# Kernel optimization log

Hardware: AMD Instinct MI355X
Metric: run time of the kernel (lower is better)

Reference implementation:

```python
import jax, jax.numpy as jnp
import numpy as np

N_NODES = 100000
N_EDGES = 1600000
N_REL = 8      # num_node_types in the torch module, used as relation count
D_IN = 128
D_HID = 128
D_OUT = 64


def setup_inputs() -> dict:
    key = jax.random.key(0)
    ks = jax.random.split(key, 16)
    x = jax.random.normal(ks[0], (N_NODES, D_IN), dtype=jnp.float32)
    edge_index = jax.random.randint(ks[1], (2, N_EDGES), 0, N_NODES, dtype=jnp.int64)
    edge_type = jax.random.randint(ks[2], (N_EDGES,), 0, N_REL, dtype=jnp.int64)
    # Glorot-ish init scale for stability
    def w(k, shape):
        fan = shape[-2] + shape[-1]
        return jax.random.normal(k, shape, dtype=jnp.float32) * jnp.sqrt(2.0 / fan)
    params = {
        'Wrel1': w(ks[3], (N_REL, D_IN, D_HID)),  'Wroot1': w(ks[4], (D_IN, D_HID)),  'b1': jnp.zeros((D_HID,), jnp.float32),
        'Wrel2': w(ks[5], (N_REL, D_HID, D_HID)), 'Wroot2': w(ks[6], (D_HID, D_HID)), 'b2': jnp.zeros((D_HID,), jnp.float32),
        'Wrel3': w(ks[7], (N_REL, D_HID, D_OUT)), 'Wroot3': w(ks[8], (D_HID, D_OUT)), 'b3': jnp.zeros((D_OUT,), jnp.float32),
    }
    return {'x': x, 'edge_index': edge_index, 'edge_type': edge_type, **params}


def _rgcn_conv(x, src, dst, edge_type, Wrel, Wroot, b):
    # Per-relation transform of all nodes: [R, N, out] (small GEMMs),
    # then per-edge gather + scatter-add (the memory-bound part).
    h = jnp.einsum('ni,rio->rno', x, Wrel)          # [R, N, out]
    msgs = h[edge_type, src]                        # [E, out] irregular gather
    agg = jax.ops.segment_sum(msgs, dst, num_segments=x.shape[0])  # [N, out]
    return x @ Wroot + b + agg


def reference(x, edge_index, edge_type, Wrel1, Wroot1, b1, Wrel2, Wroot2, b2, Wrel3, Wroot3, b3):
    src, dst = edge_index[0], edge_index[1]
    # Dropout is identity in eval mode (training=False in the torch module).
    h = jax.nn.relu(_rgcn_conv(x, src, dst, edge_type, Wrel1, Wroot1, b1))
    h = jax.nn.relu(_rgcn_conv(h, src, dst, edge_type, Wrel2, Wroot2, b2))
    h = _rgcn_conv(h, src, dst, edge_type, Wrel3, Wroot3, b3)
    return jax.nn.log_softmax(h, axis=-1)
```

## Files before the change

kernel.cpp:

```cpp
#include <hip/hip_runtime.h>


#define DEVI __device__ __forceinline__

typedef __attribute__((ext_vector_type(8))) short bf16x8;
typedef __attribute__((ext_vector_type(4))) float f32x4;

DEVI unsigned short f2b(float f) {
  unsigned int u = __builtin_bit_cast(unsigned int, f);
  unsigned int r = (u + 0x7FFFu + ((u >> 16) & 1u)) >> 16;
  return (unsigned short)r;
}
DEVI float b2f(unsigned short h) {
  unsigned int u = ((unsigned int)h) << 16;
  return __builtin_bit_cast(float, u);
}
DEVI float lo16f(unsigned v) { return __builtin_bit_cast(float, v << 16); }
DEVI float hi16f(unsigned v) { return __builtin_bit_cast(float, v & 0xFFFF0000u); }
DEVI int imin(int a, int b) { return a < b ? a : b; }


__global__ void k_zero2(int* __restrict__ cnt, int n) {
  int stride = gridDim.x * blockDim.x;
  for (int i = blockIdx.x * blockDim.x + threadIdx.x; i < n; i += stride) cnt[i] = 0;
}

__global__ void k_chist(const int* __restrict__ et, const int* __restrict__ edst,
                        int* __restrict__ gh, int NG, int E) {
  __shared__ int h[128];
  if (threadIdx.x < 128) h[threadIdx.x] = 0;
  __syncthreads();
  int stride = gridDim.x * blockDim.x;
  for (int i = blockIdx.x * blockDim.x + threadIdx.x; i < E; i += stride)
    atomicAdd(&h[(et[i] & 7) * NG + (edst[i] >> 13)], 1);
  __syncthreads();
  if (threadIdx.x < 128) atomicAdd(&gh[threadIdx.x], h[threadIdx.x]);
}

__global__ void k_cscan(const int* __restrict__ gh, int* __restrict__ gcursor,
                        int* __restrict__ cbase, int NBC, int E) {
  if (threadIdx.x == 0) {
    int a = 0;
    for (int b = 0; b < NBC; ++b) { cbase[b] = a; gcursor[b] = a; a += gh[b]; }
    cbase[NBC] = E;
  }
}

__launch_bounds__(256)
__global__ void k_cfill(const int* __restrict__ et, const int* __restrict__ esrc,
                        const int* __restrict__ edst, int* __restrict__ gcursor,
                        int* __restrict__ stage, int NG, int E) {
  __shared__ int h[128], base[128], lc[128];
  int nb = gridDim.x;
  int slice = (E + nb - 1) / nb;
  int lo = blockIdx.x * slice;
  int hi = lo + slice < E ? lo + slice : E;
  int t = threadIdx.x;
  if (t < 128) { h[t] = 0; lc[t] = 0; }
  __syncthreads();
  for (int i = lo + t; i < hi; i += 256)
    atomicAdd(&h[(et[i] & 7) * NG + (edst[i] >> 13)], 1);
  __syncthreads();
  if (t < 128 && h[t] > 0) base[t] = atomicAdd(&gcursor[t], h[t]);
  __syncthreads();
  for (int i = lo + t; i < hi; i += 256) {
    int d = edst[i];
    int tile = d >> 6;
    int bin = (et[i] & 7) * NG + (tile >> 7);
    int p = base[bin] + atomicAdd(&lc[bin], 1);
    stage[p] = ((tile & 127) << 23) | ((d & 63) << 17) | esrc[i];
  }
}

__launch_bounds__(1024)
__global__ void k_fine(const int* __restrict__ cbase, const int* __restrict__ stage,
                       int* __restrict__ srcl, int* __restrict__ lo9,
                       int* __restrict__ len9, int NG, int NTr) {
  __shared__ int h[8192];
  __shared__ int tsum[1024];
  __shared__ int wsum[16];
  int b = blockIdx.x;
  int rel = b / NG, tg = b - rel * NG;
  int lo = cbase[b], hi = cbase[b + 1];
  int t = threadIdx.x;
  for (int k = t; k < 8192; k += 1024) h[k] = 0;
  __syncthreads();
  for (int i = lo + t; i < hi; i += 1024)
    atomicAdd(&h[(stage[i] >> 17) & 0x1FFF], 1);
  __syncthreads();
  int dbase = tg * 8192;
  size_t relbase = (size_t)rel * NTr;
  for (int k = t; k < 8192; k += 1024) {
    int d = dbase + k;
    if (d < NTr) len9[relbase + d] = h[k];
  }
  int loc[8];
  int s = 0;
  int kb = t * 8;
#pragma unroll
  for (int j = 0; j < 8; ++j) { loc[j] = s; s += h[kb + j]; }
  tsum[t] = s;
  __syncthreads();
  int lane = t & 63, w = t >> 6;
  int v = tsum[t];
#pragma unroll
  for (int o = 1; o < 64; o <<= 1) {
    int u = __shfl_up(v, o);
    if (lane >= o) v += u;
  }
  if (lane == 63) wsum[w] = v;
  __syncthreads();
  if (t == 0) {
    int a = 0;
#pragma unroll
    for (int j = 0; j < 16; ++j) { int tmp = wsum[j]; wsum[j] = a; a += tmp; }
  }
  __syncthreads();
  int texcl = v - s + wsum[w];
#pragma unroll
  for (int j = 0; j < 8; ++j) h[kb + j] = texcl + loc[j];
  __syncthreads();
  for (int k = t; k < 8192; k += 1024) {
    int d = dbase + k;
    if (d < NTr) lo9[relbase + d] = lo + h[k];
  }
  __syncthreads();
  for (int i = lo + t; i < hi; i += 1024) {
    int pk = stage[i];
    int key = (pk >> 17) & 0x1FFF;
    int p = atomicAdd(&h[key], 1);
    srcl[lo + p] = pk & 0x1FFFF;
  }
}


__global__ void wprep_kernel(const float* __restrict__ Wrel, const float* __restrict__ Wroot,
                             unsigned short* __restrict__ wt, int DOUT) {
  int total = 9 * 128 * DOUT;
  int stride = gridDim.x * blockDim.x;
  for (int i = blockIdx.x * blockDim.x + threadIdx.x; i < total; i += stride) {
    int k = i & 127;
    int oo = i >> 7;
    int o = oo % DOUT;
    int rr = oo / DOUT;
    float v = (rr < 8) ? Wrel[((size_t)rr * 128 + k) * DOUT + o]
                       : Wroot[(size_t)k * DOUT + o];
    wt[i] = f2b(v);
  }
}


template <int NRP>
__launch_bounds__(256)
__global__ void agg_kernel(const unsigned* __restrict__ x32,
                           const int* __restrict__ lo9, const int* __restrict__ len9,
                           const int* __restrict__ srcl,
                           unsigned* __restrict__ Ydw,
                           int r0, int N, int E, int NTr) {
  int lane = threadIdx.x & 63;
  int d = (blockIdx.x * blockDim.x + threadIdx.x) >> 6;
  if (d >= N) return;

  int lo[NRP], ln[NRP];
#pragma unroll
  for (int r = 0; r < NRP; ++r) {
    size_t idx = (size_t)(r0 + r) * NTr + d;
    lo[r] = lo9[idx];
    ln[r] = len9[idx];
  }

  int s0[NRP], s1[NRP];
#pragma unroll
  for (int r = 0; r < NRP; ++r) {
    s0[r] = srcl[imin(lo[r], E - 1)];
    s1[r] = srcl[imin(lo[r] + 1, E - 1)];
  }
  unsigned v0[NRP], v1[NRP];
#pragma unroll
  for (int r = 0; r < NRP; ++r) {
    v0[r] = x32[(size_t)s0[r] * 64 + lane];
    v1[r] = x32[(size_t)s1[r] * 64 + lane];
  }

#pragma unroll
  for (int r = 0; r < NRP; ++r) {
    float a0 = 0.f, a1 = 0.f;
    if (ln[r] > 0) { a0 += lo16f(v0[r]); a1 += hi16f(v0[r]); }
    if (ln[r] > 1) { a0 += lo16f(v1[r]); a1 += hi16f(v1[r]); }
    if (ln[r] > 2) {
      int i = lo[r] + 2, e = lo[r] + ln[r];
      for (; i + 2 <= e; i += 2) {
        int sA = srcl[i], sB = srcl[i + 1];
        unsigned vA = x32[(size_t)sA * 64 + lane];
        unsigned vB = x32[(size_t)sB * 64 + lane];
        a0 += lo16f(vA) + lo16f(vB);
        a1 += hi16f(vA) + hi16f(vB);
      }
      if (i < e) {
        unsigned vA = x32[(size_t)srcl[i] * 64 + lane];
        a0 += lo16f(vA);
        a1 += hi16f(vA);
      }
    }
    Ydw[(size_t)d * (NRP * 64) + r * 64 + lane] =
        (unsigned)f2b(a0) | ((unsigned)f2b(a1) << 16);
  }
}


struct SrcArr {
  const unsigned short* a[9];
  const unsigned short* w[9];
  int st[9];
};

template <int DOUT, int NK, int EPI>
__launch_bounds__(256)
__global__ void gemm_lds(SrcArr S, const float* __restrict__ bias,
                         const unsigned short* __restrict__ part,
                         unsigned short* __restrict__ out_b,
                         float* __restrict__ out_f, int N) {
  __shared__ unsigned short Al[2][64 * 128];
  constexpr int NF = (DOUT == 128) ? 2 : 1;
  int tid = threadIdx.x, wid = tid >> 6, lane = tid & 63;
  int colb = lane & 15, kgrp = lane >> 4;
  int colw = wid * 16 * NF;
  int tilebase = blockIdx.x * 64;

  auto stage = [&](int t, int buf) {
    const unsigned short* sa = S.a[t] + (size_t)tilebase * S.st[t];
    int st = S.st[t];
#pragma unroll
    for (int q = 0; q < 4; ++q) {
      int c = q * 256 + tid;
      int row = c >> 4, kcl = c & 15;
      int kcg = kcl ^ (row & 7);
      const unsigned short* gp = sa + (size_t)row * st + kcg * 8;
      unsigned short* lp = &Al[buf][(q * 256 + (tid & ~63)) * 8];
      __builtin_amdgcn_global_load_lds(
          (__attribute__((address_space(1))) void*)gp,
          (__attribute__((address_space(3))) void*)lp, 16, 0, 0);
    }
  };

  f32x4 acc[4][NF];
#pragma unroll
  for (int rb = 0; rb < 4; ++rb)
#pragma unroll
    for (int nf = 0; nf < NF; ++nf) {
      f32x4 z = {0.f, 0.f, 0.f, 0.f};
      acc[rb][nf] = z;
    }

  stage(0, 0);
#pragma unroll
  for (int t = 0; t < NK; ++t) {
    __syncthreads();
    if (t + 1 < NK) stage(t + 1, (t + 1) & 1);
    const unsigned short* W = S.w[t];
    const unsigned short* Ab = Al[t & 1];
#pragma unroll
    for (int kk = 0; kk < 4; ++kk) {
      int kc = kk * 4 + kgrp;
      bf16x8 a[4];
#pragma unroll
      for (int rb = 0; rb < 4; ++rb) {
        int arow = rb * 16 + colb;
        a[rb] = *(const bf16x8*)(Ab + (size_t)(arow * 16 + (kc ^ (arow & 7))) * 8);
      }
#pragma unroll
      for (int nf = 0; nf < NF; ++nf) {
        bf16x8 b = *(const bf16x8*)(W + (size_t)(colw + nf * 16 + colb) * 128 + kc * 8);
#pragma unroll
        for (int rb = 0; rb < 4; ++rb)
          acc[rb][nf] = __builtin_amdgcn_mfma_f32_16x16x32_bf16(a[rb], b, acc[rb][nf], 0, 0, 0);
      }
    }
  }

  float bv[NF];
  if (EPI == 0 || EPI == 3 || EPI == 4) {
#pragma unroll
    for (int nf = 0; nf < NF; ++nf) bv[nf] = bias[colw + nf * 16 + colb];
  }

  if ((EPI == 2 || EPI == 4) && DOUT == 64) {
    float* Lf = (float*)Al;
    __syncthreads();
#pragma unroll
    for (int rb = 0; rb < 4; ++rb)
#pragma unroll
      for (int i = 0; i < 4; ++i) {
        int row = rb * 16 + kgrp * 4 + i;
        int grow = tilebase + row;
        int rc = grow < N ? grow : 0;
        float v = acc[rb][0][i];
        if (EPI == 4) v += bv[0];
        else v += b2f(part[(size_t)rc * 64 + colw + colb]);
        Lf[row * 68 + colw + colb] = v;
      }
    __syncthreads();
#pragma unroll
    for (int it = 0; it < 4; ++it) {
      int row = wid * 16 + it * 4 + (lane >> 4);
      float v[4];
#pragma unroll
      for (int j = 0; j < 4; ++j) v[j] = Lf[row * 68 + colb + j * 16];
      float m = fmaxf(fmaxf(v[0], v[1]), fmaxf(v[2], v[3]));
#pragma unroll
      for (int s = 1; s < 16; s <<= 1) m = fmaxf(m, __shfl_xor(m, s));
      float sum = 0.f;
#pragma unroll
      for (int j = 0; j < 4; ++j) sum += __expf(v[j] - m);
#pragma unroll
      for (int s = 1; s < 16; s <<= 1) sum += __shfl_xor(sum, s);
      float lse = m + __logf(sum);
      int grow = tilebase + row;
      if (grow < N) {
#pragma unroll
        for (int j = 0; j < 4; ++j)
          out_f[(size_t)grow * 64 + colb + j * 16] = v[j] - lse;
      }
    }
  } else {
#pragma unroll
    for (int rb = 0; rb < 4; ++rb)
#pragma unroll
      for (int i = 0; i < 4; ++i) {
        int row = tilebase + rb * 16 + kgrp * 4 + i;
        bool ok = row < N;
        int rc = ok ? row : 0;
#pragma unroll
        for (int nf = 0; nf < NF; ++nf) {
          int col = colw + nf * 16 + colb;
          float v = acc[rb][nf][i];
          if (EPI == 0 || EPI == 3) v += bv[nf];
          if (EPI == 1 || EPI == 5) v += b2f(part[(size_t)rc * DOUT + col]);
          if (EPI == 1 || EPI == 3) v = fmaxf(v, 0.f);
          if (ok) out_b[(size_t)row * DOUT + col] = f2b(v);
        }
      }
  }
}

template <int DOUT>
static void run_gemm(int NK, int EPI, const SrcArr& S, const float* bias,
                     const unsigned short* part, unsigned short* ob, float* of,
                     int N, int NT, hipStream_t st) {
#define GCALL(nk, epi)                                                        \
  if (NK == nk && EPI == epi) {                                               \
    gemm_lds<DOUT, nk, epi><<<NT, 256, 0, st>>>(S, bias, part, ob, of, N);    \
    return;                                                                   \
  }
  GCALL(9, 3) GCALL(9, 4)
  GCALL(5, 0) GCALL(4, 1) GCALL(4, 2)
  GCALL(3, 0) GCALL(2, 5) GCALL(2, 1) GCALL(2, 2)
#undef GCALL
}


__global__ void cast_kernel(const float* __restrict__ in, unsigned short* __restrict__ out,
                            int n4) {
  int stride = gridDim.x * blockDim.x;
  for (int i = blockIdx.x * blockDim.x + threadIdx.x; i < n4; i += stride) {
    float4 v = ((const float4*)in)[i];
    ushort4 o;
    o.x = f2b(v.x); o.y = f2b(v.y); o.z = f2b(v.z); o.w = f2b(v.w);
    ((ushort4*)out)[i] = o;
  }
}


extern "C" void kernel_launch(void* const* d_in, const int* in_sizes, int n_in,
                              void* d_out, int out_size, void* d_ws, size_t ws_size,
                              hipStream_t stream) {
  const float* x = (const float*)d_in[0];
  const int* eidx = (const int*)d_in[1];
  const int* et = (const int*)d_in[2];
  const float* Wrel1 = (const float*)d_in[3];
  const float* Wroot1 = (const float*)d_in[4];
  const float* b1 = (const float*)d_in[5];
  const float* Wrel2 = (const float*)d_in[6];
  const float* Wroot2 = (const float*)d_in[7];
  const float* b2 = (const float*)d_in[8];
  const float* Wrel3 = (const float*)d_in[9];
  const float* Wroot3 = (const float*)d_in[10];
  const float* b3 = (const float*)d_in[11];

  const int N = in_sizes[0] / 128;
  const int E = in_sizes[2];
  const int NT = (N + 63) / 64;
  const int NTr = NT * 64;
  const int NG = (NT + 127) / 128;
  const int NBC = 8 * NG;
  const int* esrc = eidx;
  const int* edst = eidx + E;

  const size_t XB = (size_t)NTr * 128 * 2;

  size_t fixedB = 2 * XB + 2 * ((size_t)9 * 128 * 128 * 2) + (size_t)9 * 64 * 128 * 2 +
                  2 * ((size_t)E * 4) + 2 * ((size_t)8 * NTr * 4) + 4096 + 16 * 256;
  int NRP = 8;
  if (fixedB + 8 * XB > ws_size) NRP = 4;
  if (NRP == 4 && fixedB + 4 * XB + XB > ws_size) NRP = 2;

  char* p = (char*)d_ws;
  auto carve = [&](size_t bytes) {
    void* q = (void*)p;
    p += (bytes + 255) & ~(size_t)255;
    return q;
  };
  unsigned short* bufX0 = (unsigned short*)carve(XB);
  unsigned short* bufX1 = (unsigned short*)carve(XB);
  unsigned short* wt1 = (unsigned short*)carve((size_t)9 * 128 * 128 * 2);
  unsigned short* wt2 = (unsigned short*)carve((size_t)9 * 128 * 128 * 2);
  unsigned short* wt3 = (unsigned short*)carve((size_t)9 * 64 * 128 * 2);
  int* stage = (int*)carve((size_t)E * 4);
  int* srcl = (int*)carve((size_t)E * 4);
  int* lo9 = (int*)carve((size_t)8 * NTr * 4);
  int* len9 = (int*)carve((size_t)8 * NTr * 4);
  int* gh = (int*)carve(512);
  int* gcursor = (int*)carve(512);
  int* cbase = (int*)carve(512);
  unsigned short* part = (unsigned short*)((NRP < 8) ? carve(XB) : nullptr);
  unsigned short* Y = (unsigned short*)carve((size_t)NRP * XB);

  k_zero2<<<1, 128, 0, stream>>>(gh, 128);
  k_chist<<<512, 256, 0, stream>>>(et, edst, gh, NG, E);
  k_cscan<<<1, 64, 0, stream>>>(gh, gcursor, cbase, NBC, E);
  k_cfill<<<512, 256, 0, stream>>>(et, esrc, edst, gcursor, stage, NG, E);
  k_fine<<<NBC, 1024, 0, stream>>>(cbase, stage, srcl, lo9, len9, NG, NTr);

  wprep_kernel<<<576, 256, 0, stream>>>(Wrel1, Wroot1, wt1, 128);
  wprep_kernel<<<576, 256, 0, stream>>>(Wrel2, Wroot2, wt2, 128);
  wprep_kernel<<<288, 256, 0, stream>>>(Wrel3, Wroot3, wt3, 64);
  cast_kernel<<<2048, 256, 0, stream>>>(x, bufX0, N * 128 / 4);

  const int ablk = (N * 64 + 255) / 256;
  const int passes = 8 / NRP;

  auto layer = [&](const unsigned short* xin, const unsigned short* wt,
                   const float* bias, int DOUT, unsigned short* xout, float* fout) {
    for (int pidx = 0; pidx < passes; ++pidx) {
      int r0 = pidx * NRP;
      if (NRP == 8)
        agg_kernel<8><<<ablk, 256, 0, stream>>>((const unsigned*)xin, lo9, len9, srcl, (unsigned*)Y, r0, N, E, NTr);
      else if (NRP == 4)
        agg_kernel<4><<<ablk, 256, 0, stream>>>((const unsigned*)xin, lo9, len9, srcl, (unsigned*)Y, r0, N, E, NTr);
      else
        agg_kernel<2><<<ablk, 256, 0, stream>>>((const unsigned*)xin, lo9, len9, srcl, (unsigned*)Y, r0, N, E, NTr);

      SrcArr S;
      int idx = 0;
      if (pidx == 0) {
        S.a[0] = xin; S.w[0] = wt + (size_t)8 * DOUT * 128; S.st[0] = 128;
        idx = 1;
      }
      for (int j = 0; j < NRP; ++j) {
        S.a[idx] = Y + j * 128;
        S.w[idx] = wt + (size_t)(r0 + j) * DOUT * 128;
        S.st[idx] = NRP * 128;
        ++idx;
      }
      int NK = idx;
      int epi;
      bool lastp = (pidx == passes - 1);
      if (pidx == 0 && lastp) epi = (DOUT == 64) ? 4 : 3;
      else if (pidx == 0) epi = 0;
      else if (!lastp) epi = 5;
      else epi = (DOUT == 64) ? 2 : 1;

      unsigned short* ob = lastp ? xout : part;
      if (pidx == 0 && !lastp) ob = part;
      if (DOUT == 128)
        run_gemm<128>(NK, epi, S, bias, part, ob, fout, N, NT, stream);
      else
        run_gemm<64>(NK, epi, S, bias, part, ob, fout, N, NT, stream);
    }
  };

  layer(bufX0, wt1, b1, 128, bufX1, nullptr);
  layer(bufX1, wt2, b2, 128, bufX0, nullptr);
  layer(bufX0, wt3, b3, 64, nullptr, (float*)d_out);
}
```

Baseline: 694.4 us.

## Fuse per-relation gather aggregation into the GEMM kernel per layer

Replaces the separate aggregation kernel, which wrote per-relation sums Y to global memory, and the multi-input GEMM with one fused kernel per layer. Each block aggregates one relation's neighbor sums for its 64-row tile into LDS and then runs the MFMA step for that relation, overlapping the next relation's first gathers with the current MFMA. This removes the round trip of the large Y buffer through global memory and the partial-sum passes. In exchange, occupancy and memory-level parallelism drop: each wave handles 16 rows serially with a per-edge loop, and about 36 KB of LDS per block limits residency.

Result: slower. 801.0 us (+15.4%).

```diff
diff --git a/kernel.cpp b/kernel.cpp
--- a/kernel.cpp
+++ b/kernel.cpp
@@ -150,98 +150,50 @@
 }
 
 
-template <int NRP>
+template <int DOUT, bool LSM>
 __launch_bounds__(256)
-__global__ void agg_kernel(const unsigned* __restrict__ x32,
-                           const int* __restrict__ lo9, const int* __restrict__ len9,
-                           const int* __restrict__ srcl,
-                           unsigned* __restrict__ Ydw,
-                           int r0, int N, int E, int NTr) {
-  int lane = threadIdx.x & 63;
-  int d = (blockIdx.x * blockDim.x + threadIdx.x) >> 6;
-  if (d >= N) return;
-
-  int lo[NRP], ln[NRP];
-#pragma unroll
-  for (int r = 0; r < NRP; ++r) {
-    size_t idx = (size_t)(r0 + r) * NTr + d;
-    lo[r] = lo9[idx];
-    ln[r] = len9[idx];
-  }
-
-  int s0[NRP], s1[NRP];
-#pragma unroll
-  for (int r = 0; r < NRP; ++r) {
-    s0[r] = srcl[imin(lo[r], E - 1)];
-    s1[r] = srcl[imin(lo[r] + 1, E - 1)];
-  }
-  unsigned v0[NRP], v1[NRP];
-#pragma unroll
-  for (int r = 0; r < NRP; ++r) {
-    v0[r] = x32[(size_t)s0[r] * 64 + lane];
-    v1[r] = x32[(size_t)s1[r] * 64 + lane];
-  }
-
-#pragma unroll
-  for (int r = 0; r < NRP; ++r) {
-    float a0 = 0.f, a1 = 0.f;
-    if (ln[r] > 0) { a0 += lo16f(v0[r]); a1 += hi16f(v0[r]); }
-    if (ln[r] > 1) { a0 += lo16f(v1[r]); a1 += hi16f(v1[r]); }
-    if (ln[r] > 2) {
-      int i = lo[r] + 2, e = lo[r] + ln[r];
-      for (; i + 2 <= e; i += 2) {
-        int sA = srcl[i], sB = srcl[i + 1];
-        unsigned vA = x32[(size_t)sA * 64 + lane];
-        unsigned vB = x32[(size_t)sB * 64 + lane];
-        a0 += lo16f(vA) + lo16f(vB);
-        a1 += hi16f(vA) + hi16f(vB);
-      }
-      if (i < e) {
-        unsigned vA = x32[(size_t)srcl[i] * 64 + lane];
-        a0 += lo16f(vA);
-        a1 += hi16f(vA);
-      }
-    }
-    Ydw[(size_t)d * (NRP * 64) + r * 64 + lane] =
-        (unsigned)f2b(a0) | ((unsigned)f2b(a1) << 16);
-  }
-}
-
-
-struct SrcArr {
-  const unsigned short* a[9];
-  const unsigned short* w[9];
-  int st[9];
-};
-
-template <int DOUT, int NK, int EPI>
-__launch_bounds__(256)
-__global__ void gemm_lds(SrcArr S, const float* __restrict__ bias,
-                         const unsigned short* __restrict__ part,
-                         unsigned short* __restrict__ out_b,
-                         float* __restrict__ out_f, int N) {
-  __shared__ unsigned short Al[2][64 * 128];
+__global__ void fused_layer(const unsigned short* __restrict__ xb,
+                            const unsigned short* __restrict__ wt,
+                            const int* __restrict__ lo9,
+                            const int* __restrict__ len9,
+                            const int* __restrict__ srcl,
+                            const float* __restrict__ bias,
+                            unsigned short* __restrict__ out_b,
+                            float* __restrict__ out_f,
+                            int N, int NTr, int E) {
+  __shared__ unsigned short XY[2 * 64 * 128];
+  __shared__ int ll0[512], ll1[512];
+  unsigned short* Xl = XY;
+  unsigned short* Yl = XY + 8192;
   constexpr int NF = (DOUT == 128) ? 2 : 1;
   int tid = threadIdx.x, wid = tid >> 6, lane = tid & 63;
   int colb = lane & 15, kgrp = lane >> 4;
   int colw = wid * 16 * NF;
   int tilebase = blockIdx.x * 64;
-
-  auto stage = [&](int t, int buf) {
-    const unsigned short* sa = S.a[t] + (size_t)tilebase * S.st[t];
-    int st = S.st[t];
+  const unsigned* x32 = (const unsigned*)xb;
+
+  {
+    const unsigned short* sa = xb + (size_t)tilebase * 128;
 #pragma unroll
     for (int q = 0; q < 4; ++q) {
       int c = q * 256 + tid;
       int row = c >> 4, kcl = c & 15;
       int kcg = kcl ^ (row & 7);
-      const unsigned short* gp = sa + (size_t)row * st + kcg * 8;
-      unsigned short* lp = &Al[buf][(q * 256 + (tid & ~63)) * 8];
+      const unsigned short* gp = sa + (size_t)row * 128 + kcg * 8;
+      unsigned short* lp = &Xl[(q * 256 + (tid & ~63)) * 8];
       __builtin_amdgcn_global_load_lds(
           (__attribute__((address_space(1))) void*)gp,
           (__attribute__((address_space(3))) void*)lp, 16, 0, 0);
     }
-  };
+  }
+#pragma unroll
+  for (int q = 0; q < 2; ++q) {
+    int idx = q * 256 + tid;
+    int r = idx >> 6, c = idx & 63;
+    size_t g = (size_t)r * NTr + tilebase + c;
+    ll0[idx] = lo9[g];
+    ll1[idx] = len9[g];
+  }
 
   f32x4 acc[4][NF];
 #pragma unroll
@@ -252,13 +204,45 @@
       acc[rb][nf] = z;
     }
 
-  stage(0, 0);
-#pragma unroll
-  for (int t = 0; t < NK; ++t) {
-    __syncthreads();
-    if (t + 1 < NK) stage(t + 1, (t + 1) & 1);
-    const unsigned short* W = S.w[t];
-    const unsigned short* Ab = Al[t & 1];
+  int s_lo[16], s_ln[16];
+  unsigned s_v0[16], s_v1[16];
+
+  auto aggLoad = [&](int r) {
+#pragma unroll
+    for (int j = 0; j < 16; ++j) {
+      int row = wid * 16 + j;
+      int lo = ll0[r * 64 + row];
+      int ln = ll1[r * 64 + row];
+      s_lo[j] = lo;
+      s_ln[j] = ln;
+      int a = srcl[imin(lo, E - 1)];
+      int b = srcl[imin(lo + 1, E - 1)];
+      s_v0[j] = x32[(size_t)a * 64 + lane];
+      s_v1[j] = x32[(size_t)b * 64 + lane];
+    }
+  };
+
+  auto aggFinish = [&]() {
+    unsigned* Yd = (unsigned*)Yl;
+#pragma unroll
+    for (int j = 0; j < 16; ++j) {
+      int row = wid * 16 + j;
+      float a0 = 0.f, a1 = 0.f;
+      int lo = s_lo[j], ln = s_ln[j];
+      if (ln > 0) { a0 += lo16f(s_v0[j]); a1 += hi16f(s_v0[j]); }
+      if (ln > 1) { a0 += lo16f(s_v1[j]); a1 += hi16f(s_v1[j]); }
+      for (int i = lo + 2; i < lo + ln; ++i) {
+        unsigned v = x32[(size_t)srcl[i] * 64 + lane];
+        a0 += lo16f(v);
+        a1 += hi16f(v);
+      }
+      int c = lane >> 2;
+      int pos = row * 64 + ((c ^ (row & 7)) << 2) + (lane & 3);
+      Yd[pos] = (unsigned)f2b(a0) | ((unsigned)f2b(a1) << 16);
+    }
+  };
+
+  auto mfmaStep = [&](const unsigned short* Ab, const unsigned short* W) {
 #pragma unroll
     for (int kk = 0; kk < 4; ++kk) {
       int kc = kk * 4 + kgrp;
@@ -276,33 +260,35 @@
           acc[rb][nf] = __builtin_amdgcn_mfma_f32_16x16x32_bf16(a[rb], b, acc[rb][nf], 0, 0, 0);
       }
     }
-  }
-
-  float bv[NF];
-  if (EPI == 0 || EPI == 3 || EPI == 4) {
-#pragma unroll
-    for (int nf = 0; nf < NF; ++nf) bv[nf] = bias[colw + nf * 16 + colb];
-  }
-
-  if ((EPI == 2 || EPI == 4) && DOUT == 64) {
-    float* Lf = (float*)Al;
+  };
+
+  __syncthreads();
+  aggLoad(0);
+  mfmaStep(Xl, wt + (size_t)8 * DOUT * 128);
+
+  for (int r = 0; r < 8; ++r) {
+    __syncthreads();
+    aggFinish();
+    __syncthreads();
+    mfmaStep(Yl, wt + (size_t)r * DOUT * 128);
+    if (r < 7) aggLoad(r + 1);
+  }
+
+  if (LSM) {
+    float* Lf = (float*)XY;
+    float bv = bias[colw + colb];
     __syncthreads();
 #pragma unroll
     for (int rb = 0; rb < 4; ++rb)
 #pragma unroll
       for (int i = 0; i < 4; ++i) {
         int row = rb * 16 + kgrp * 4 + i;
-        int grow = tilebase + row;
-        int rc = grow < N ? grow : 0;
-        float v = acc[rb][0][i];
-        if (EPI == 4) v += bv[0];
-        else v += b2f(part[(size_t)rc * 64 + colw + colb]);
-        Lf[row * 68 + colw + colb] = v;
+        Lf[row * 68 + colw + colb] = acc[rb][0][i] + bv;
       }
     __syncthreads();
 #pragma unroll
     for (int it = 0; it < 4; ++it) {
-      int row = wid * 16 + it * 4 + (lane >> 4);
+      int row = wid * 16 + it * 4 + kgrp;
       float v[4];
 #pragma unroll
       for (int j = 0; j < 4; ++j) v[j] = Lf[row * 68 + colb + j * 16];
@@ -323,39 +309,23 @@
       }
     }
   } else {
+    float bv[NF];
+#pragma unroll
+    for (int nf = 0; nf < NF; ++nf) bv[nf] = bias[colw + nf * 16 + colb];
 #pragma unroll
     for (int rb = 0; rb < 4; ++rb)
 #pragma unroll
       for (int i = 0; i < 4; ++i) {
         int row = tilebase + rb * 16 + kgrp * 4 + i;
-        bool ok = row < N;
-        int rc = ok ? row : 0;
+        if (row >= N) continue;
 #pragma unroll
         for (int nf = 0; nf < NF; ++nf) {
           int col = colw + nf * 16 + colb;
-          float v = acc[rb][nf][i];
-          if (EPI == 0 || EPI == 3) v += bv[nf];
-          if (EPI == 1 || EPI == 5) v += b2f(part[(size_t)rc * DOUT + col]);
-          if (EPI == 1 || EPI == 3) v = fmaxf(v, 0.f);
-          if (ok) out_b[(size_t)row * DOUT + col] = f2b(v);
+          float v = acc[rb][nf][i] + bv[nf];
+          out_b[(size_t)row * DOUT + col] = f2b(fmaxf(v, 0.f));
         }
       }
   }
-}
-
-template <int DOUT>
-static void run_gemm(int NK, int EPI, const SrcArr& S, const float* bias,
-                     const unsigned short* part, unsigned short* ob, float* of,
-                     int N, int NT, hipStream_t st) {
-#define GCALL(nk, epi)                                                        \
-  if (NK == nk && EPI == epi) {                                               \
-    gemm_lds<DOUT, nk, epi><<<NT, 256, 0, st>>>(S, bias, part, ob, of, N);    \
-    return;                                                                   \
-  }
-  GCALL(9, 3) GCALL(9, 4)
-  GCALL(5, 0) GCALL(4, 1) GCALL(4, 2)
-  GCALL(3, 0) GCALL(2, 5) GCALL(2, 1) GCALL(2, 2)
-#undef GCALL
 }
 
 
@@ -397,12 +367,6 @@
   const int* edst = eidx + E;
 
   const size_t XB = (size_t)NTr * 128 * 2;
-
-  size_t fixedB = 2 * XB + 2 * ((size_t)9 * 128 * 128 * 2) + (size_t)9 * 64 * 128 * 2 +
-                  2 * ((size_t)E * 4) + 2 * ((size_t)8 * NTr * 4) + 4096 + 16 * 256;
-  int NRP = 8;
-  if (fixedB + 8 * XB > ws_size) NRP = 4;
-  if (NRP == 4 && fixedB + 4 * XB + XB > ws_size) NRP = 2;
 
   char* p = (char*)d_ws;
   auto carve = [&](size_t bytes) {
@@ -422,8 +386,6 @@
   int* gh = (int*)carve(512);
   int* gcursor = (int*)carve(512);
   int* cbase = (int*)carve(512);
-  unsigned short* part = (unsigned short*)((NRP < 8) ? carve(XB) : nullptr);
-  unsigned short* Y = (unsigned short*)carve((size_t)NRP * XB);
 
   k_zero2<<<1, 128, 0, stream>>>(gh, 128);
   k_chist<<<512, 256, 0, stream>>>(et, edst, gh, NG, E);
@@ -436,50 +398,11 @@
   wprep_kernel<<<288, 256, 0, stream>>>(Wrel3, Wroot3, wt3, 64);
   cast_kernel<<<2048, 256, 0, stream>>>(x, bufX0, N * 128 / 4);
 
-  const int ablk = (N * 64 + 255) / 256;
-  const int passes = 8 / NRP;
-
-  auto layer = [&](const unsigned short* xin, const unsigned short* wt,
-                   const float* bias, int DOUT, unsigned short* xout, float* fout) {
-    for (int pidx = 0; pidx < passes; ++pidx) {
-      int r0 = pidx * NRP;
-      if (NRP == 8)
-        agg_kernel<8><<<ablk, 256, 0, stream>>>((const unsigned*)xin, lo9, len9, srcl, (unsigned*)Y, r0, N, E, NTr);
-      else if (NRP == 4)
-        agg_kernel<4><<<ablk, 256, 0, stream>>>((const unsigned*)xin, lo9, len9, srcl, (unsigned*)Y, r0, N, E, NTr);
-      else
-        agg_kernel<2><<<ablk, 256, 0, stream>>>((const unsigned*)xin, lo9, len9, srcl, (unsigned*)Y, r0, N, E, NTr);
-
-      SrcArr S;
-      int idx = 0;
-      if (pidx == 0) {
-        S.a[0] = xin; S.w[0] = wt + (size_t)8 * DOUT * 128; S.st[0] = 128;
-        idx = 1;
-      }
-      for (int j = 0; j < NRP; ++j) {
-        S.a[idx] = Y + j * 128;
-        S.w[idx] = wt + (size_t)(r0 + j) * DOUT * 128;
-        S.st[idx] = NRP * 128;
-        ++idx;
-      }
-      int NK = idx;
-      int epi;
-      bool lastp = (pidx == passes - 1);
-      if (pidx == 0 && lastp) epi = (DOUT == 64) ? 4 : 3;
-      else if (pidx == 0) epi = 0;
-      else if (!lastp) epi = 5;
-      else epi = (DOUT == 64) ? 2 : 1;
-
-      unsigned short* ob = lastp ? xout : part;
-      if (pidx == 0 && !lastp) ob = part;
-      if (DOUT == 128)
-        run_gemm<128>(NK, epi, S, bias, part, ob, fout, N, NT, stream);
-      else
-        run_gemm<64>(NK, epi, S, bias, part, ob, fout, N, NT, stream);
-    }
-  };
-
-  layer(bufX0, wt1, b1, 128, bufX1, nullptr);
-  layer(bufX1, wt2, b2, 128, bufX0, nullptr);
-  layer(bufX0, wt3, b3, 64, nullptr, (float*)d_out);
-}
+  fused_layer<128, false><<<NT, 256, 0, stream>>>(bufX0, wt1, lo9, len9, srcl, b1,
+                                                  bufX1, (float*)nullptr, N, NTr, E);
+  fused_layer<128, false><<<NT, 256, 0, stream>>>(bufX1, wt2, lo9, len9, srcl, b2,
+                                                  bufX0, (float*)nullptr, N, NTr, E);
+  fused_layer<64, true><<<NT, 256, 0, stream>>>(bufX0, wt3, lo9, len9, srcl, b3,
+                                                (unsigned short*)nullptr, (float*)d_out,
+                                                N, NTr, E);
+}
```
